# Kernel optimization log

Hardware: AMD Instinct MI355X
Metric: run time of the kernel (lower is better)

Reference implementation:

```python
import jax, jax.numpy as jnp
import numpy as np


def setup_inputs() -> dict:
    key = jax.random.key(0)
    x = jax.random.normal(key, (8, 2048, 512), dtype=jnp.float32)
    return {"x": x}


def reference(x):
    # x: [B, S, D]; unscaled causal self-attention with Q=K=V=x
    B, S, D = x.shape
    scores = jnp.einsum('bsd,btd->bst', x, x)  # [B, S, S]
    causal = jnp.tril(jnp.ones((S, S), dtype=bool))  # True where allowed
    scores = jnp.where(causal[None, :, :], scores, -jnp.inf)
    attn = jax.nn.softmax(scores, axis=-1)
    out = jnp.einsum('bst,btd->bsd', attn, x)  # [B, S, D]
    return out
```

## Files before the change

kernel.cpp:

```cpp
#include <hip/hip_runtime.h>


#define S_LEN 2048
#define D_DIM 512
#define BATCH_ELEMS 1048576

typedef short s16x8 __attribute__((ext_vector_type(8)));
typedef float f32x4 __attribute__((ext_vector_type(4)));

__device__ __forceinline__ unsigned short f2b_rne(float f) {
  unsigned int u = __float_as_uint(f);
  return (unsigned short)((u + 0x7FFFu + ((u >> 16) & 1u)) >> 16);
}
__device__ __forceinline__ unsigned short f2b_fast(float f) {
  return (unsigned short)((__float_as_uint(f) + 0x8000u) >> 16);
}

template <int CTRL>
__device__ __forceinline__ float dppf(float x) {
  return __uint_as_float((unsigned)__builtin_amdgcn_update_dpp(
      0, (int)__float_as_uint(x), CTRL, 0xF, 0xF, true));
}
__device__ __forceinline__ float red16_max(float v) {
  v = fmaxf(v, dppf<0xB1>(v));
  v = fmaxf(v, dppf<0x4E>(v));
  v = fmaxf(v, dppf<0x124>(v));
  v = fmaxf(v, dppf<0x128>(v));
  return v;
}
__device__ __forceinline__ float red16_sum(float v) {
  v += dppf<0xB1>(v);
  v += dppf<0x4E>(v);
  v += dppf<0x124>(v);
  v += dppf<0x128>(v);
  return v;
}

__global__ void pack_kernel(const float* __restrict__ x,
                            unsigned short* __restrict__ Kf,
                            unsigned short* __restrict__ Vf) {
  __shared__ unsigned short A[64 * 72];
  __shared__ unsigned short T[64 * 72];
  const int bid = blockIdx.x;
  const int b = bid >> 8, rem = bid & 255;
  const int s0 = (rem >> 3) * 64, d0 = (rem & 7) * 64;
  const int tid = threadIdx.x;

  #pragma unroll
  for (int it = 0; it < 2; ++it) {
    int slot = it * 256 + tid;
    int row = slot >> 3, c = slot & 7;
    const float* src = x + ((size_t)(b * S_LEN + s0 + row)) * D_DIM + d0 + c * 8;
    const float4 v0 = *(const float4*)(src);
    const float4 v1 = *(const float4*)(src + 4);
    s16x8 o;
    o[0] = (short)f2b_rne(v0.x); o[1] = (short)f2b_rne(v0.y);
    o[2] = (short)f2b_rne(v0.z); o[3] = (short)f2b_rne(v0.w);
    o[4] = (short)f2b_rne(v1.x); o[5] = (short)f2b_rne(v1.y);
    o[6] = (short)f2b_rne(v1.z); o[7] = (short)f2b_rne(v1.w);
    *(s16x8*)&A[row * 72 + c * 8] = o;
  }
  __syncthreads();

  {
    int sr = tid >> 4, sc = tid & 15;
    ushort4 a0 = *(const ushort4*)&A[(4 * sr + 0) * 72 + 4 * sc];
    ushort4 a1 = *(const ushort4*)&A[(4 * sr + 1) * 72 + 4 * sc];
    ushort4 a2 = *(const ushort4*)&A[(4 * sr + 2) * 72 + 4 * sc];
    ushort4 a3 = *(const ushort4*)&A[(4 * sr + 3) * 72 + 4 * sc];
    ushort4 t0; t0.x = a0.x; t0.y = a1.x; t0.z = a2.x; t0.w = a3.x;
    ushort4 t1; t1.x = a0.y; t1.y = a1.y; t1.z = a2.y; t1.w = a3.y;
    ushort4 t2; t2.x = a0.z; t2.y = a1.z; t2.z = a2.z; t2.w = a3.z;
    ushort4 t3; t3.x = a0.w; t3.y = a1.w; t3.z = a2.w; t3.w = a3.w;
    *(ushort4*)&T[(4 * sc + 0) * 72 + 4 * sr] = t0;
    *(ushort4*)&T[(4 * sc + 1) * 72 + 4 * sr] = t1;
    *(ushort4*)&T[(4 * sc + 2) * 72 + 4 * sr] = t2;
    *(ushort4*)&T[(4 * sc + 3) * 72 + 4 * sr] = t3;
  }
  __syncthreads();

  #pragma unroll
  for (int it = 0; it < 2; ++it) {
    int slot = it * 256 + tid;
    int frag = slot >> 6;
    int lane = slot & 63;
    int l15 = lane & 15, quad = lane >> 4;
    int f1 = frag >> 1, f0 = frag & 1;
    {
      s16x8 val = *(const s16x8*)&A[(f1 * 16 + l15) * 72 + f0 * 32 + quad * 8];
      size_t kg = (size_t)(s0 >> 4) + f1, db = (size_t)(d0 >> 5) + f0;
      *(s16x8*)(Kf + (size_t)b * BATCH_ELEMS + (kg * 16 + db) * 512 + lane * 8) = val;
    }
    {
      s16x8 val = *(const s16x8*)&T[(f1 * 16 + l15) * 72 + f0 * 32 + quad * 8];
      size_t dg = (size_t)(d0 >> 4) + f1, kb = (size_t)(s0 >> 5) + f0;
      *(s16x8*)(Vf + (size_t)b * BATCH_ELEMS + (dg * 64 + kb) * 512 + lane * 8) = val;
    }
  }
}

__global__ __launch_bounds__(256, 3)
void attn_kernel(const unsigned short* __restrict__ Kf,
                 const unsigned short* __restrict__ Vf,
                 float* __restrict__ out) {
  __shared__ float Xc[2][4][512];
  __shared__ unsigned short Pw[4][16 * 40];

  const int bid = blockIdx.x;
  const int bat = bid & 7;
  const int rg = 127 - (bid >> 3);
  const int q0 = rg * 16;
  const int tmax = rg >> 1;
  const int tid = threadIdx.x;
  const int w = tid >> 6;
  const int lane = tid & 63;
  const int l15 = lane & 15, quad = lane >> 4;
  const size_t batOff = (size_t)bat * BATCH_ELEMS;

  s16x8 kreg[8];
  auto loadK = [&](int kt) {
    const unsigned short* kb = Kf + batOff + (size_t)kt * 16384 + lane * 8;
    #pragma unroll
    for (int i = 0; i < 4; ++i) {
      kreg[i]     = *(const s16x8*)(kb + (size_t)(w * 4 + i) * 512);
      kreg[4 + i] = *(const s16x8*)(kb + (size_t)(16 + w * 4 + i) * 512);
    }
  };

  s16x8 vreg[8];
  auto loadV = [&](int kt) {
    const unsigned short* vb = Vf + batOff + (size_t)kt * 512 + lane * 8;
    #pragma unroll
    for (int dgl = 0; dgl < 8; ++dgl)
      vreg[dgl] = *(const s16x8*)(vb + (size_t)(w * 8 + dgl) * 32768);
  };

  loadK(0);
  loadV(0);

  s16x8 qf[4];
  {
    const unsigned short* qb =
        Kf + batOff + ((size_t)rg * 16 + w * 4) * 512 + lane * 8;
    #pragma unroll
    for (int i = 0; i < 4; ++i) qf[i] = *(const s16x8*)(qb + i * 512);
  }

  f32x4 O[8];
  float m[4], l[4];
  #pragma unroll
  for (int n = 0; n < 8; ++n) O[n] = (f32x4){0.f, 0.f, 0.f, 0.f};
  #pragma unroll
  for (int r = 0; r < 4; ++r) { m[r] = -3e38f; l[r] = 0.f; }

  for (int kt = 0;; ++kt) {
    const int p = kt & 1;

    f32x4 sacc[2];
    sacc[0] = (f32x4){0.f, 0.f, 0.f, 0.f};
    sacc[1] = (f32x4){0.f, 0.f, 0.f, 0.f};
    __builtin_amdgcn_s_setprio(1);
    #pragma unroll
    for (int i = 0; i < 4; ++i) {
      sacc[0] = __builtin_amdgcn_mfma_f32_16x16x32_bf16(qf[i], kreg[i], sacc[0], 0, 0, 0);
      sacc[1] = __builtin_amdgcn_mfma_f32_16x16x32_bf16(qf[i], kreg[4 + i], sacc[1], 0, 0, 0);
    }
    __builtin_amdgcn_s_setprio(0);

    if (kt < tmax) loadK(kt + 1);

    *(f32x4*)&Xc[p][w][lane * 4] = sacc[0];
    *(f32x4*)&Xc[p][w][256 + lane * 4] = sacc[1];
    asm volatile("s_waitcnt lgkmcnt(0)" ::: "memory");
    __builtin_amdgcn_s_barrier();
    __builtin_amdgcn_sched_barrier(0);
    {
      f32x4 s0 = (f32x4){0.f, 0.f, 0.f, 0.f};
      f32x4 s1 = (f32x4){0.f, 0.f, 0.f, 0.f};
      #pragma unroll
      for (int ww = 0; ww < 4; ++ww) {
        if (ww == w) {
          s0 += sacc[0];
          s1 += sacc[1];
        } else {
          s0 += *(const f32x4*)&Xc[p][ww][lane * 4];
          s1 += *(const f32x4*)&Xc[p][ww][256 + lane * 4];
        }
      }
      sacc[0] = s0;
      sacc[1] = s1;
    }

    if (kt == tmax) {
      #pragma unroll
      for (int kg2 = 0; kg2 < 2; ++kg2)
        #pragma unroll
        for (int r = 0; r < 4; ++r) {
          int key = kt * 32 + kg2 * 16 + l15;
          int row = q0 + quad * 4 + r;
          if (key > row) sacc[kg2][r] = -3e38f;
        }
    }

    float mt[4], alpha[4];
    #pragma unroll
    for (int r = 0; r < 4; ++r)
      mt[r] = red16_max(fmaxf(sacc[0][r], sacc[1][r]));
    bool needAny = (mt[0] > m[0] + 8.f) | (mt[1] > m[1] + 8.f) |
                   (mt[2] > m[2] + 8.f) | (mt[3] > m[3] + 8.f);
    unsigned long long bal = __ballot(needAny);
    if (bal) {
      #pragma unroll
      for (int r = 0; r < 4; ++r) {
        float mn = fmaxf(m[r], mt[r]);
        alpha[r] = __expf(m[r] - mn);
        m[r] = mn;
      }
    } else {
      #pragma unroll
      for (int r = 0; r < 4; ++r) alpha[r] = 1.0f;
    }
    float p2[2][4];
    #pragma unroll
    for (int kg2 = 0; kg2 < 2; ++kg2)
      #pragma unroll
      for (int r = 0; r < 4; ++r) p2[kg2][r] = __expf(sacc[kg2][r] - m[r]);
    #pragma unroll
    for (int r = 0; r < 4; ++r)
      l[r] = l[r] * alpha[r] + red16_sum(p2[0][r] + p2[1][r]);

    #pragma unroll
    for (int kg2 = 0; kg2 < 2; ++kg2)
      #pragma unroll
      for (int r = 0; r < 4; ++r)
        Pw[w][(quad * 4 + r) * 40 + kg2 * 16 + l15] = f2b_fast(p2[kg2][r]);
    s16x8 pa = *(const s16x8*)&Pw[w][l15 * 40 + quad * 8];

    if (bal) {
      #pragma unroll
      for (int n = 0; n < 8; ++n)
        #pragma unroll
        for (int r = 0; r < 4; ++r) O[n][r] *= alpha[r];
    }

    __builtin_amdgcn_s_setprio(1);
    #pragma unroll
    for (int dgl = 0; dgl < 8; ++dgl)
      O[dgl] = __builtin_amdgcn_mfma_f32_16x16x32_bf16(pa, vreg[dgl], O[dgl], 0, 0, 0);
    __builtin_amdgcn_s_setprio(0);

    if (kt == tmax) break;

    loadV(kt + 1);
  }

  float invl[4];
  #pragma unroll
  for (int r = 0; r < 4; ++r) invl[r] = 1.0f / l[r];
  float* ob = out + ((size_t)(bat * S_LEN + q0)) * D_DIM + w * 128;
  #pragma unroll
  for (int dgl = 0; dgl < 8; ++dgl)
    #pragma unroll
    for (int r = 0; r < 4; ++r)
      ob[(size_t)(quad * 4 + r) * D_DIM + dgl * 16 + l15] = O[dgl][r] * invl[r];
}

extern "C" void kernel_launch(void* const* d_in, const int* in_sizes, int n_in,
                              void* d_out, int out_size, void* d_ws, size_t ws_size,
                              hipStream_t stream) {
  (void)in_sizes; (void)n_in; (void)out_size; (void)ws_size;
  const float* x = (const float*)d_in[0];
  float* out = (float*)d_out;
  unsigned short* Kf = (unsigned short*)d_ws;
  unsigned short* Vf = (unsigned short*)((char*)d_ws + (16u << 20));
  pack_kernel<<<2048, 256, 0, stream>>>(x, Kf, Vf);
  attn_kernel<<<1024, 256, 0, stream>>>(Kf, Vf, out);
}
```

Before: 173.5 us.

## Process 32 query rows per block to reuse K/V tiles across two row groups

Each block now handles two 16-row query groups (32 rows) against each 32-key tile, so each K and V fragment loaded from global memory feeds twice as many MFMAs and the grid shrinks to 512 blocks. Softmax statistics for the two row groups are computed by waves 0 and 3 only, then shared through LDS as probabilities, alpha rescale factors and flags, which adds a second barrier per iteration. The V packing layout changes so each wave's V slice for a key tile is contiguous, and the block ordering puts long causal tiles first, then short ones. More accumulator registers lower occupancy to 2 blocks per SM, and idle waves during softmax can reduce overlap.

```diff
diff --git a/kernel.cpp b/kernel.cpp
--- a/kernel.cpp
+++ b/kernel.cpp
@@ -94,175 +94,216 @@
     {
       s16x8 val = *(const s16x8*)&T[(f1 * 16 + l15) * 72 + f0 * 32 + quad * 8];
       size_t dg = (size_t)(d0 >> 4) + f1, kb = (size_t)(s0 >> 5) + f0;
-      *(s16x8*)(Vf + (size_t)b * BATCH_ELEMS + (dg * 64 + kb) * 512 + lane * 8) = val;
-    }
-  }
-}
-
-__global__ __launch_bounds__(256, 3)
+      *(s16x8*)(Vf + (size_t)b * BATCH_ELEMS + (kb * 32 + dg) * 512 + lane * 8) = val;
+    }
+  }
+}
+
+__global__ __launch_bounds__(256, 2)
 void attn_kernel(const unsigned short* __restrict__ Kf,
                  const unsigned short* __restrict__ Vf,
                  float* __restrict__ out) {
-  __shared__ float Xc[2][4][512];
-  __shared__ unsigned short Pw[4][16 * 40];
+  __shared__ float Xc[2][4][1024];
+  __shared__ unsigned short Pw[2][32 * 40];
+  __shared__ float alphaBuf[2][32];
+  __shared__ int flagBuf[2][2];
+  __shared__ float lBuf[32];
 
   const int bid = blockIdx.x;
   const int bat = bid & 7;
-  const int rg = 127 - (bid >> 3);
-  const int q0 = rg * 16;
-  const int tmax = rg >> 1;
+  const int t = (bid < 256) ? (63 - (bid >> 3)) : ((bid - 256) >> 3);
+  const int q0 = t * 32;
+  const int tmax = t;
   const int tid = threadIdx.x;
   const int w = tid >> 6;
   const int lane = tid & 63;
   const int l15 = lane & 15, quad = lane >> 4;
   const size_t batOff = (size_t)bat * BATCH_ELEMS;
-
-  s16x8 kreg[8];
+  const int srg = (w == 0) ? 0 : ((w == 3) ? 1 : -1);
+
+  s16x8 kreg[2][4];
   auto loadK = [&](int kt) {
-    const unsigned short* kb = Kf + batOff + (size_t)kt * 16384 + lane * 8;
-    #pragma unroll
-    for (int i = 0; i < 4; ++i) {
-      kreg[i]     = *(const s16x8*)(kb + (size_t)(w * 4 + i) * 512);
-      kreg[4 + i] = *(const s16x8*)(kb + (size_t)(16 + w * 4 + i) * 512);
-    }
+    const unsigned short* kb =
+        Kf + batOff + (size_t)kt * 16384 + (size_t)(w * 4) * 512 + lane * 8;
+    #pragma unroll
+    for (int g = 0; g < 2; ++g)
+      #pragma unroll
+      for (int i = 0; i < 4; ++i)
+        kreg[g][i] = *(const s16x8*)(kb + (size_t)(g * 16 + i) * 512);
   };
 
   s16x8 vreg[8];
   auto loadV = [&](int kt) {
-    const unsigned short* vb = Vf + batOff + (size_t)kt * 512 + lane * 8;
-    #pragma unroll
-    for (int dgl = 0; dgl < 8; ++dgl)
-      vreg[dgl] = *(const s16x8*)(vb + (size_t)(w * 8 + dgl) * 32768);
+    const unsigned short* vb =
+        Vf + batOff + ((size_t)kt * 32 + w * 8) * 512 + lane * 8;
+    #pragma unroll
+    for (int d = 0; d < 8; ++d)
+      vreg[d] = *(const s16x8*)(vb + (size_t)d * 512);
   };
 
   loadK(0);
   loadV(0);
 
-  s16x8 qf[4];
+  s16x8 qf[2][4];
   {
     const unsigned short* qb =
-        Kf + batOff + ((size_t)rg * 16 + w * 4) * 512 + lane * 8;
-    #pragma unroll
-    for (int i = 0; i < 4; ++i) qf[i] = *(const s16x8*)(qb + i * 512);
-  }
-
-  f32x4 O[8];
+        Kf + batOff + ((size_t)(2 * t) * 16 + w * 4) * 512 + lane * 8;
+    #pragma unroll
+    for (int rg = 0; rg < 2; ++rg)
+      #pragma unroll
+      for (int i = 0; i < 4; ++i)
+        qf[rg][i] = *(const s16x8*)(qb + (size_t)(rg * 16 + i) * 512);
+  }
+
+  f32x4 O[2][8];
+  #pragma unroll
+  for (int rg = 0; rg < 2; ++rg)
+    #pragma unroll
+    for (int d = 0; d < 8; ++d) O[rg][d] = (f32x4){0.f, 0.f, 0.f, 0.f};
   float m[4], l[4];
-  #pragma unroll
-  for (int n = 0; n < 8; ++n) O[n] = (f32x4){0.f, 0.f, 0.f, 0.f};
   #pragma unroll
   for (int r = 0; r < 4; ++r) { m[r] = -3e38f; l[r] = 0.f; }
 
   for (int kt = 0;; ++kt) {
     const int p = kt & 1;
 
-    f32x4 sacc[2];
-    sacc[0] = (f32x4){0.f, 0.f, 0.f, 0.f};
-    sacc[1] = (f32x4){0.f, 0.f, 0.f, 0.f};
+    f32x4 sacc[2][2];
+    #pragma unroll
+    for (int rg = 0; rg < 2; ++rg)
+      #pragma unroll
+      for (int g = 0; g < 2; ++g) sacc[rg][g] = (f32x4){0.f, 0.f, 0.f, 0.f};
     __builtin_amdgcn_s_setprio(1);
     #pragma unroll
     for (int i = 0; i < 4; ++i) {
-      sacc[0] = __builtin_amdgcn_mfma_f32_16x16x32_bf16(qf[i], kreg[i], sacc[0], 0, 0, 0);
-      sacc[1] = __builtin_amdgcn_mfma_f32_16x16x32_bf16(qf[i], kreg[4 + i], sacc[1], 0, 0, 0);
+      sacc[0][0] = __builtin_amdgcn_mfma_f32_16x16x32_bf16(qf[0][i], kreg[0][i], sacc[0][0], 0, 0, 0);
+      sacc[0][1] = __builtin_amdgcn_mfma_f32_16x16x32_bf16(qf[0][i], kreg[1][i], sacc[0][1], 0, 0, 0);
+      sacc[1][0] = __builtin_amdgcn_mfma_f32_16x16x32_bf16(qf[1][i], kreg[0][i], sacc[1][0], 0, 0, 0);
+      sacc[1][1] = __builtin_amdgcn_mfma_f32_16x16x32_bf16(qf[1][i], kreg[1][i], sacc[1][1], 0, 0, 0);
     }
     __builtin_amdgcn_s_setprio(0);
 
     if (kt < tmax) loadK(kt + 1);
 
-    *(f32x4*)&Xc[p][w][lane * 4] = sacc[0];
-    *(f32x4*)&Xc[p][w][256 + lane * 4] = sacc[1];
+    #pragma unroll
+    for (int rg = 0; rg < 2; ++rg)
+      #pragma unroll
+      for (int g = 0; g < 2; ++g)
+        *(f32x4*)&Xc[p][w][(rg * 2 + g) * 256 + lane * 4] = sacc[rg][g];
     asm volatile("s_waitcnt lgkmcnt(0)" ::: "memory");
     __builtin_amdgcn_s_barrier();
     __builtin_amdgcn_sched_barrier(0);
+
+    if (srg >= 0) {
+      f32x4 s0 = sacc[srg][0], s1 = sacc[srg][1];
+      #pragma unroll
+      for (int ww = 0; ww < 4; ++ww) {
+        if (ww != w) {
+          s0 += *(const f32x4*)&Xc[p][ww][(srg * 2 + 0) * 256 + lane * 4];
+          s1 += *(const f32x4*)&Xc[p][ww][(srg * 2 + 1) * 256 + lane * 4];
+        }
+      }
+      if (kt == tmax) {
+        #pragma unroll
+        for (int r = 0; r < 4; ++r) {
+          int row = srg * 16 + quad * 4 + r;
+          if (l15 > row) s0[r] = -3e38f;
+          if (16 + l15 > row) s1[r] = -3e38f;
+        }
+      }
+      float mt[4], alpha[4];
+      #pragma unroll
+      for (int r = 0; r < 4; ++r) mt[r] = red16_max(fmaxf(s0[r], s1[r]));
+      bool needAny = (mt[0] > m[0] + 8.f) | (mt[1] > m[1] + 8.f) |
+                     (mt[2] > m[2] + 8.f) | (mt[3] > m[3] + 8.f);
+      unsigned long long bal = __ballot(needAny);
+      if (bal) {
+        #pragma unroll
+        for (int r = 0; r < 4; ++r) {
+          float mn = fmaxf(m[r], mt[r]);
+          alpha[r] = __expf(m[r] - mn);
+          m[r] = mn;
+        }
+      }
+      float e0[4], e1[4];
+      #pragma unroll
+      for (int r = 0; r < 4; ++r) {
+        e0[r] = __expf(s0[r] - m[r]);
+        e1[r] = __expf(s1[r] - m[r]);
+      }
+      #pragma unroll
+      for (int r = 0; r < 4; ++r) {
+        float lp = bal ? l[r] * alpha[r] : l[r];
+        l[r] = lp + red16_sum(e0[r] + e1[r]);
+      }
+      #pragma unroll
+      for (int r = 0; r < 4; ++r) {
+        int row = srg * 16 + quad * 4 + r;
+        Pw[p][row * 40 + l15] = f2b_fast(e0[r]);
+        Pw[p][row * 40 + 16 + l15] = f2b_fast(e1[r]);
+      }
+      if (bal) {
+        #pragma unroll
+        for (int r = 0; r < 4; ++r)
+          alphaBuf[p][srg * 16 + quad * 4 + r] = alpha[r];
+      }
+      if (lane == 0) flagBuf[p][srg] = bal ? 1 : 0;
+    }
+    asm volatile("s_waitcnt lgkmcnt(0)" ::: "memory");
+    __builtin_amdgcn_s_barrier();
+    __builtin_amdgcn_sched_barrier(0);
+
     {
-      f32x4 s0 = (f32x4){0.f, 0.f, 0.f, 0.f};
-      f32x4 s1 = (f32x4){0.f, 0.f, 0.f, 0.f};
-      #pragma unroll
-      for (int ww = 0; ww < 4; ++ww) {
-        if (ww == w) {
-          s0 += sacc[0];
-          s1 += sacc[1];
-        } else {
-          s0 += *(const f32x4*)&Xc[p][ww][lane * 4];
-          s1 += *(const f32x4*)&Xc[p][ww][256 + lane * 4];
-        }
-      }
-      sacc[0] = s0;
-      sacc[1] = s1;
-    }
-
-    if (kt == tmax) {
-      #pragma unroll
-      for (int kg2 = 0; kg2 < 2; ++kg2)
-        #pragma unroll
-        for (int r = 0; r < 4; ++r) {
-          int key = kt * 32 + kg2 * 16 + l15;
-          int row = q0 + quad * 4 + r;
-          if (key > row) sacc[kg2][r] = -3e38f;
-        }
-    }
-
-    float mt[4], alpha[4];
+      int f0 = flagBuf[p][0];
+      int f1 = flagBuf[p][1];
+      if (f0) {
+        f32x4 a = *(const f32x4*)&alphaBuf[p][quad * 4];
+        #pragma unroll
+        for (int d = 0; d < 8; ++d)
+          #pragma unroll
+          for (int r = 0; r < 4; ++r) O[0][d][r] *= a[r];
+      }
+      if (f1) {
+        f32x4 a = *(const f32x4*)&alphaBuf[p][16 + quad * 4];
+        #pragma unroll
+        for (int d = 0; d < 8; ++d)
+          #pragma unroll
+          for (int r = 0; r < 4; ++r) O[1][d][r] *= a[r];
+      }
+    }
+
+    s16x8 pa0 = *(const s16x8*)&Pw[p][l15 * 40 + quad * 8];
+    s16x8 pa1 = *(const s16x8*)&Pw[p][(16 + l15) * 40 + quad * 8];
+    __builtin_amdgcn_s_setprio(1);
+    #pragma unroll
+    for (int d = 0; d < 8; ++d)
+      O[0][d] = __builtin_amdgcn_mfma_f32_16x16x32_bf16(pa0, vreg[d], O[0][d], 0, 0, 0);
+    #pragma unroll
+    for (int d = 0; d < 8; ++d)
+      O[1][d] = __builtin_amdgcn_mfma_f32_16x16x32_bf16(pa1, vreg[d], O[1][d], 0, 0, 0);
+    __builtin_amdgcn_s_setprio(0);
+
+    if (kt == tmax) break;
+    loadV(kt + 1);
+  }
+
+  if (srg >= 0) {
     #pragma unroll
     for (int r = 0; r < 4; ++r)
-      mt[r] = red16_max(fmaxf(sacc[0][r], sacc[1][r]));
-    bool needAny = (mt[0] > m[0] + 8.f) | (mt[1] > m[1] + 8.f) |
-                   (mt[2] > m[2] + 8.f) | (mt[3] > m[3] + 8.f);
-    unsigned long long bal = __ballot(needAny);
-    if (bal) {
-      #pragma unroll
-      for (int r = 0; r < 4; ++r) {
-        float mn = fmaxf(m[r], mt[r]);
-        alpha[r] = __expf(m[r] - mn);
-        m[r] = mn;
-      }
-    } else {
-      #pragma unroll
-      for (int r = 0; r < 4; ++r) alpha[r] = 1.0f;
-    }
-    float p2[2][4];
-    #pragma unroll
-    for (int kg2 = 0; kg2 < 2; ++kg2)
-      #pragma unroll
-      for (int r = 0; r < 4; ++r) p2[kg2][r] = __expf(sacc[kg2][r] - m[r]);
-    #pragma unroll
-    for (int r = 0; r < 4; ++r)
-      l[r] = l[r] * alpha[r] + red16_sum(p2[0][r] + p2[1][r]);
-
-    #pragma unroll
-    for (int kg2 = 0; kg2 < 2; ++kg2)
-      #pragma unroll
-      for (int r = 0; r < 4; ++r)
-        Pw[w][(quad * 4 + r) * 40 + kg2 * 16 + l15] = f2b_fast(p2[kg2][r]);
-    s16x8 pa = *(const s16x8*)&Pw[w][l15 * 40 + quad * 8];
-
-    if (bal) {
-      #pragma unroll
-      for (int n = 0; n < 8; ++n)
-        #pragma unroll
-        for (int r = 0; r < 4; ++r) O[n][r] *= alpha[r];
-    }
-
-    __builtin_amdgcn_s_setprio(1);
-    #pragma unroll
-    for (int dgl = 0; dgl < 8; ++dgl)
-      O[dgl] = __builtin_amdgcn_mfma_f32_16x16x32_bf16(pa, vreg[dgl], O[dgl], 0, 0, 0);
-    __builtin_amdgcn_s_setprio(0);
-
-    if (kt == tmax) break;
-
-    loadV(kt + 1);
-  }
-
-  float invl[4];
-  #pragma unroll
-  for (int r = 0; r < 4; ++r) invl[r] = 1.0f / l[r];
+      lBuf[srg * 16 + quad * 4 + r] = 1.0f / l[r];
+  }
+  asm volatile("s_waitcnt lgkmcnt(0)" ::: "memory");
+  __builtin_amdgcn_s_barrier();
+  __builtin_amdgcn_sched_barrier(0);
+  f32x4 il0 = *(const f32x4*)&lBuf[quad * 4];
+  f32x4 il1 = *(const f32x4*)&lBuf[16 + quad * 4];
   float* ob = out + ((size_t)(bat * S_LEN + q0)) * D_DIM + w * 128;
   #pragma unroll
-  for (int dgl = 0; dgl < 8; ++dgl)
-    #pragma unroll
-    for (int r = 0; r < 4; ++r)
-      ob[(size_t)(quad * 4 + r) * D_DIM + dgl * 16 + l15] = O[dgl][r] * invl[r];
+  for (int d = 0; d < 8; ++d)
+    #pragma unroll
+    for (int r = 0; r < 4; ++r) {
+      ob[(size_t)(quad * 4 + r) * D_DIM + d * 16 + l15] = O[0][d][r] * il0[r];
+      ob[(size_t)(16 + quad * 4 + r) * D_DIM + d * 16 + l15] = O[1][d][r] * il1[r];
+    }
 }
 
 extern "C" void kernel_launch(void* const* d_in, const int* in_sizes, int n_in,
@@ -274,5 +315,5 @@
   unsigned short* Kf = (unsigned short*)d_ws;
   unsigned short* Vf = (unsigned short*)((char*)d_ws + (16u << 20));
   pack_kernel<<<2048, 256, 0, stream>>>(x, Kf, Vf);
-  attn_kernel<<<1024, 256, 0, stream>>>(Kf, Vf, out);
-}
+  attn_kernel<<<512, 256, 0, stream>>>(Kf, Vf, out);
+}
```

Result: slower. 239.1 us (+37.8%).

## Widen key tile to 64 per iteration, relayout K/V, compute row sums via MFMA

Applied to the files above, without the earlier changes.

The key tile per loop iteration grows from 32 to 64 keys, so each barrier and cross-wave score reduction and each online-softmax update covers twice as many keys. The packed K and V layouts change so that each wave's K and V fragments for a tile sit contiguously in memory. The DPP row-sum reduction is replaced by an MFMA against a vector of ones, which accumulates the softmax denominator on the matrix unit. More registers are needed, so launch bounds drop from 3 to 2 blocks per SM, which costs occupancy.

```diff
diff --git a/kernel.cpp b/kernel.cpp
--- a/kernel.cpp
+++ b/kernel.cpp
@@ -26,13 +26,6 @@
   v = fmaxf(v, dppf<0x4E>(v));
   v = fmaxf(v, dppf<0x124>(v));
   v = fmaxf(v, dppf<0x128>(v));
-  return v;
-}
-__device__ __forceinline__ float red16_sum(float v) {
-  v += dppf<0xB1>(v);
-  v += dppf<0x4E>(v);
-  v += dppf<0x124>(v);
-  v += dppf<0x128>(v);
   return v;
 }
 
@@ -88,51 +81,60 @@
     int f1 = frag >> 1, f0 = frag & 1;
     {
       s16x8 val = *(const s16x8*)&A[(f1 * 16 + l15) * 72 + f0 * 32 + quad * 8];
-      size_t kg = (size_t)(s0 >> 4) + f1, db = (size_t)(d0 >> 5) + f0;
-      *(s16x8*)(Kf + (size_t)b * BATCH_ELEMS + (kg * 16 + db) * 512 + lane * 8) = val;
+      size_t kg = (size_t)(s0 >> 4) + f1;
+      int db = (d0 >> 5) + f0;
+      size_t dq = (size_t)(db >> 2), dbl = (size_t)(db & 3);
+      *(s16x8*)(Kf + (size_t)b * BATCH_ELEMS +
+                ((dq * 128 + kg) * 4 + dbl) * 512 + lane * 8) = val;
     }
     {
       s16x8 val = *(const s16x8*)&T[(f1 * 16 + l15) * 72 + f0 * 32 + quad * 8];
       size_t dg = (size_t)(d0 >> 4) + f1, kb = (size_t)(s0 >> 5) + f0;
-      *(s16x8*)(Vf + (size_t)b * BATCH_ELEMS + (dg * 64 + kb) * 512 + lane * 8) = val;
-    }
-  }
-}
-
-__global__ __launch_bounds__(256, 3)
+      *(s16x8*)(Vf + (size_t)b * BATCH_ELEMS + (kb * 32 + dg) * 512 + lane * 8) = val;
+    }
+  }
+}
+
+__global__ __launch_bounds__(256, 2)
 void attn_kernel(const unsigned short* __restrict__ Kf,
                  const unsigned short* __restrict__ Vf,
                  float* __restrict__ out) {
-  __shared__ float Xc[2][4][512];
-  __shared__ unsigned short Pw[4][16 * 40];
+  __shared__ float Xc[2][4][1024];
+  __shared__ unsigned short Pw[4][16 * 72];
 
   const int bid = blockIdx.x;
   const int bat = bid & 7;
   const int rg = 127 - (bid >> 3);
   const int q0 = rg * 16;
-  const int tmax = rg >> 1;
+  const int tmax = rg >> 2;
   const int tid = threadIdx.x;
   const int w = tid >> 6;
   const int lane = tid & 63;
   const int l15 = lane & 15, quad = lane >> 4;
   const size_t batOff = (size_t)bat * BATCH_ELEMS;
 
-  s16x8 kreg[8];
+  s16x8 ones;
+  #pragma unroll
+  for (int j = 0; j < 8; ++j) ones[j] = (short)0x3F80;
+
+  s16x8 kreg[16];
   auto loadK = [&](int kt) {
-    const unsigned short* kb = Kf + batOff + (size_t)kt * 16384 + lane * 8;
-    #pragma unroll
-    for (int i = 0; i < 4; ++i) {
-      kreg[i]     = *(const s16x8*)(kb + (size_t)(w * 4 + i) * 512);
-      kreg[4 + i] = *(const s16x8*)(kb + (size_t)(16 + w * 4 + i) * 512);
-    }
+    const unsigned short* kb =
+        Kf + batOff + ((size_t)(w * 128 + 4 * kt) * 4) * 512 + lane * 8;
+    #pragma unroll
+    for (int f = 0; f < 16; ++f)
+      kreg[f] = *(const s16x8*)(kb + (size_t)f * 512);
   };
 
-  s16x8 vreg[8];
+  s16x8 vreg[2][8];
   auto loadV = [&](int kt) {
-    const unsigned short* vb = Vf + batOff + (size_t)kt * 512 + lane * 8;
-    #pragma unroll
-    for (int dgl = 0; dgl < 8; ++dgl)
-      vreg[dgl] = *(const s16x8*)(vb + (size_t)(w * 8 + dgl) * 32768);
+    const unsigned short* vb =
+        Vf + batOff + ((size_t)(2 * kt) * 32 + w * 8) * 512 + lane * 8;
+    #pragma unroll
+    for (int d = 0; d < 8; ++d) {
+      vreg[0][d] = *(const s16x8*)(vb + (size_t)d * 512);
+      vreg[1][d] = *(const s16x8*)(vb + (size_t)(32 + d) * 512);
+    }
   };
 
   loadK(0);
@@ -141,9 +143,9 @@
   s16x8 qf[4];
   {
     const unsigned short* qb =
-        Kf + batOff + ((size_t)rg * 16 + w * 4) * 512 + lane * 8;
-    #pragma unroll
-    for (int i = 0; i < 4; ++i) qf[i] = *(const s16x8*)(qb + i * 512);
+        Kf + batOff + ((size_t)(w * 128 + rg) * 4) * 512 + lane * 8;
+    #pragma unroll
+    for (int i = 0; i < 4; ++i) qf[i] = *(const s16x8*)(qb + (size_t)i * 512);
   }
 
   f32x4 O[8];
@@ -156,56 +158,57 @@
   for (int kt = 0;; ++kt) {
     const int p = kt & 1;
 
-    f32x4 sacc[2];
-    sacc[0] = (f32x4){0.f, 0.f, 0.f, 0.f};
-    sacc[1] = (f32x4){0.f, 0.f, 0.f, 0.f};
+    f32x4 sacc[4];
+    #pragma unroll
+    for (int g = 0; g < 4; ++g) sacc[g] = (f32x4){0.f, 0.f, 0.f, 0.f};
     __builtin_amdgcn_s_setprio(1);
     #pragma unroll
-    for (int i = 0; i < 4; ++i) {
-      sacc[0] = __builtin_amdgcn_mfma_f32_16x16x32_bf16(qf[i], kreg[i], sacc[0], 0, 0, 0);
-      sacc[1] = __builtin_amdgcn_mfma_f32_16x16x32_bf16(qf[i], kreg[4 + i], sacc[1], 0, 0, 0);
-    }
+    for (int g = 0; g < 4; ++g)
+      #pragma unroll
+      for (int i = 0; i < 4; ++i)
+        sacc[g] = __builtin_amdgcn_mfma_f32_16x16x32_bf16(qf[i], kreg[g * 4 + i],
+                                                          sacc[g], 0, 0, 0);
     __builtin_amdgcn_s_setprio(0);
 
     if (kt < tmax) loadK(kt + 1);
 
-    *(f32x4*)&Xc[p][w][lane * 4] = sacc[0];
-    *(f32x4*)&Xc[p][w][256 + lane * 4] = sacc[1];
+    #pragma unroll
+    for (int g = 0; g < 4; ++g)
+      *(f32x4*)&Xc[p][w][g * 256 + lane * 4] = sacc[g];
     asm volatile("s_waitcnt lgkmcnt(0)" ::: "memory");
     __builtin_amdgcn_s_barrier();
     __builtin_amdgcn_sched_barrier(0);
     {
-      f32x4 s0 = (f32x4){0.f, 0.f, 0.f, 0.f};
-      f32x4 s1 = (f32x4){0.f, 0.f, 0.f, 0.f};
+      f32x4 a0[4];
+      #pragma unroll
+      for (int g = 0; g < 4; ++g) a0[g] = sacc[g];
       #pragma unroll
       for (int ww = 0; ww < 4; ++ww) {
-        if (ww == w) {
-          s0 += sacc[0];
-          s1 += sacc[1];
-        } else {
-          s0 += *(const f32x4*)&Xc[p][ww][lane * 4];
-          s1 += *(const f32x4*)&Xc[p][ww][256 + lane * 4];
-        }
+        if (ww == w) continue;
+        #pragma unroll
+        for (int g = 0; g < 4; ++g)
+          a0[g] += *(const f32x4*)&Xc[p][ww][g * 256 + lane * 4];
       }
-      sacc[0] = s0;
-      sacc[1] = s1;
+      #pragma unroll
+      for (int g = 0; g < 4; ++g) sacc[g] = a0[g];
     }
 
     if (kt == tmax) {
       #pragma unroll
-      for (int kg2 = 0; kg2 < 2; ++kg2)
+      for (int g = 0; g < 4; ++g)
         #pragma unroll
         for (int r = 0; r < 4; ++r) {
-          int key = kt * 32 + kg2 * 16 + l15;
+          int key = kt * 64 + g * 16 + l15;
           int row = q0 + quad * 4 + r;
-          if (key > row) sacc[kg2][r] = -3e38f;
+          if (key > row) sacc[g][r] = -3e38f;
         }
     }
 
     float mt[4], alpha[4];
     #pragma unroll
     for (int r = 0; r < 4; ++r)
-      mt[r] = red16_max(fmaxf(sacc[0][r], sacc[1][r]));
+      mt[r] = red16_max(fmaxf(fmaxf(sacc[0][r], sacc[1][r]),
+                              fmaxf(sacc[2][r], sacc[3][r])));
     bool needAny = (mt[0] > m[0] + 8.f) | (mt[1] > m[1] + 8.f) |
                    (mt[2] > m[2] + 8.f) | (mt[3] > m[3] + 8.f);
     unsigned long long bal = __ballot(needAny);
@@ -216,25 +219,17 @@
         alpha[r] = __expf(m[r] - mn);
         m[r] = mn;
       }
-    } else {
-      #pragma unroll
-      for (int r = 0; r < 4; ++r) alpha[r] = 1.0f;
-    }
-    float p2[2][4];
-    #pragma unroll
-    for (int kg2 = 0; kg2 < 2; ++kg2)
-      #pragma unroll
-      for (int r = 0; r < 4; ++r) p2[kg2][r] = __expf(sacc[kg2][r] - m[r]);
-    #pragma unroll
-    for (int r = 0; r < 4; ++r)
-      l[r] = l[r] * alpha[r] + red16_sum(p2[0][r] + p2[1][r]);
-
-    #pragma unroll
-    for (int kg2 = 0; kg2 < 2; ++kg2)
-      #pragma unroll
-      for (int r = 0; r < 4; ++r)
-        Pw[w][(quad * 4 + r) * 40 + kg2 * 16 + l15] = f2b_fast(p2[kg2][r]);
-    s16x8 pa = *(const s16x8*)&Pw[w][l15 * 40 + quad * 8];
+    }
+
+    #pragma unroll
+    for (int g = 0; g < 4; ++g)
+      #pragma unroll
+      for (int r = 0; r < 4; ++r) {
+        float e = __expf(sacc[g][r] - m[r]);
+        Pw[w][(quad * 4 + r) * 72 + g * 16 + l15] = f2b_fast(e);
+      }
+    s16x8 pa01 = *(const s16x8*)&Pw[w][l15 * 72 + quad * 8];
+    s16x8 pa23 = *(const s16x8*)&Pw[w][l15 * 72 + 32 + quad * 8];
 
     if (bal) {
       #pragma unroll
@@ -245,12 +240,19 @@
 
     __builtin_amdgcn_s_setprio(1);
     #pragma unroll
-    for (int dgl = 0; dgl < 8; ++dgl)
-      O[dgl] = __builtin_amdgcn_mfma_f32_16x16x32_bf16(pa, vreg[dgl], O[dgl], 0, 0, 0);
+    for (int d = 0; d < 8; ++d) {
+      O[d] = __builtin_amdgcn_mfma_f32_16x16x32_bf16(pa01, vreg[0][d], O[d], 0, 0, 0);
+      O[d] = __builtin_amdgcn_mfma_f32_16x16x32_bf16(pa23, vreg[1][d], O[d], 0, 0, 0);
+    }
+    f32x4 linc = (f32x4){0.f, 0.f, 0.f, 0.f};
+    linc = __builtin_amdgcn_mfma_f32_16x16x32_bf16(pa01, ones, linc, 0, 0, 0);
+    linc = __builtin_amdgcn_mfma_f32_16x16x32_bf16(pa23, ones, linc, 0, 0, 0);
     __builtin_amdgcn_s_setprio(0);
+    #pragma unroll
+    for (int r = 0; r < 4; ++r)
+      l[r] = (bal ? l[r] * alpha[r] : l[r]) + linc[r];
 
     if (kt == tmax) break;
-
     loadV(kt + 1);
   }
 
@@ -259,10 +261,10 @@
   for (int r = 0; r < 4; ++r) invl[r] = 1.0f / l[r];
   float* ob = out + ((size_t)(bat * S_LEN + q0)) * D_DIM + w * 128;
   #pragma unroll
-  for (int dgl = 0; dgl < 8; ++dgl)
+  for (int d = 0; d < 8; ++d)
     #pragma unroll
     for (int r = 0; r < 4; ++r)
-      ob[(size_t)(quad * 4 + r) * D_DIM + dgl * 16 + l15] = O[dgl][r] * invl[r];
+      ob[(size_t)(quad * 4 + r) * D_DIM + d * 16 + l15] = O[d][r] * invl[r];
 }
 
 extern "C" void kernel_launch(void* const* d_in, const int* in_sizes, int n_in,
```

New measurement: 161.4 us. -6.9%, faster.
